# Kernel optimization log

Hardware: AMD Instinct MI355X
Metric: run time of the kernel (lower is better)

The kernel has to match this reference:

```python
import jax, jax.numpy as jnp
import numpy as np

TAU = 0.07
EPS_NORM = 1e-12
EPS_DEN = 1e-8


def setup_inputs() -> dict:
    key = jax.random.key(0)
    k1, k2, k3, k4 = jax.random.split(key, 4)
    B, C, H, W = 2, 128, 64, 64
    return {
        "input": jax.random.normal(k1, (B, C, H, W), dtype=jnp.float32),
        "target": jax.random.normal(k2, (B, C, H, W), dtype=jnp.float32),
        "input_seg": jax.random.randint(k3, (B, H, W), 0, 4, dtype=jnp.int64 if jax.config.jax_enable_x64 else jnp.int32),
        "target_seg": jax.random.randint(k4, (B, H, W), 0, 4, dtype=jnp.int64 if jax.config.jax_enable_x64 else jnp.int32),
    }


def _flatten_normalize(x):
    # (B, C, H, W) -> (B*H*W, C), L2-normalized rows (torch F.normalize semantics)
    B, C = x.shape[0], x.shape[1]
    x = jnp.moveaxis(x, 1, -1).reshape(-1, C)
    norm = jnp.linalg.norm(x, axis=-1, keepdims=True)
    return x / jnp.maximum(norm, EPS_NORM)


def reference(input, target, input_seg, target_seg):
    ni = _flatten_normalize(input)    # (N, C)
    nt = _flatten_normalize(target)   # (N, C)
    pi = input_seg.reshape(-1)        # (N,)
    pt = target_seg.reshape(-1)       # (N,)

    # sim[a, b] = cos(target[a], input[b]); rows already unit-norm so dot == cosine
    sim = jnp.einsum("ac,bc->ab", nt, ni)
    sim_exp = jnp.exp(sim / TAU)

    # diff[a, b] = 1 if pred_input[b] != pred_target[a]
    diff = (pi[None, :] != pt[:, None]).astype(jnp.float32)

    nominator = jnp.sum((1.0 - diff) * sim_exp, axis=0)          # (N,) positives per input pixel
    denominator = jnp.sum(diff * sim_exp, axis=0) + nominator    # (N,) all pairs
    loss = -jnp.log(nominator / (denominator + EPS_DEN)).mean()
    return loss
```

## Files before the change

### kernel.cpp

```cpp
#include <hip/hip_runtime.h>

#define N_PIX 8192
#define C_DIM 128
#define TAU_INV_LOG2E 20.609929155556622f
#define EPS_DEN 1e-8f

typedef unsigned short u16;
typedef __attribute__((ext_vector_type(8))) short short8;
typedef __attribute__((ext_vector_type(4))) float f32x4;

__device__ __forceinline__ u16 f2bf(float f) {
    unsigned u = __float_as_uint(f);
    unsigned r = (u + 0x7fffu + ((u >> 16) & 1u)) >> 16;
    return (u16)r;
}

__global__ __launch_bounds__(256) void scale_k(const float* __restrict__ input,
                                               const float* __restrict__ target,
                                               float* __restrict__ scale_all) {
    int t = blockIdx.x * 256 + threadIdx.x;
    int arr = t >> 13;
    int n = t & (N_PIX - 1);
    const float* src = arr ? target : input;
    int b = n >> 12, hw = n & 4095;
    const float* p = src + b * (C_DIM * 4096) + hw;
    float ss = 0.f;
#pragma unroll 8
    for (int c = 0; c < C_DIM; ++c) {
        float v = p[c * 4096];
        ss += v * v;
    }
    scale_all[t] = 1.0f / fmaxf(sqrtf(ss), 1e-12f);
}

__global__ __launch_bounds__(256) void transpose_k(const float* __restrict__ input,
                                                   const float* __restrict__ target,
                                                   const float* __restrict__ scale_all,
                                                   u16* __restrict__ ni_bf,
                                                   u16* __restrict__ nt_bf) {
    __shared__ float tile[64][65];
    int zi = blockIdx.z;
    int arr = zi >> 1, bb = zi & 1;
    const float* src = (arr ? target : input) + bb * (C_DIM * 4096);
    u16* dst = arr ? nt_bf : ni_bf;
    int hw0 = blockIdx.x * 64;
    int c0 = blockIdx.y * 64;
    int t = threadIdx.x;
    int tq = t >> 6;
    int tl = t & 63;
#pragma unroll
    for (int i = 0; i < 16; ++i) {
        int cl = i * 4 + tq;
        tile[cl][tl] = src[(c0 + cl) * 4096 + hw0 + tl];
    }
    __syncthreads();
#pragma unroll
    for (int i = 0; i < 16; ++i) {
        int px = i * 4 + tq;
        int n = bb * 4096 + hw0 + px;
        float sc = scale_all[arr * N_PIX + n];
        dst[n * C_DIM + c0 + tl] = f2bf(tile[tl][px] * sc);
    }
}

__global__ __launch_bounds__(256, 2) void main_k(const u16* __restrict__ ni,
                                                 const u16* __restrict__ nt,
                                                 const int* __restrict__ piseg,
                                                 const int* __restrict__ ptseg,
                                                 float* __restrict__ den,
                                                 float* __restrict__ nom) {
    __shared__ __align__(16) u16 sA[128 * 136];
    __shared__ __align__(16) int spt[128];

    int bcb = blockIdx.x & 63;
    int as  = blockIdx.x >> 6;
    int bcol0 = bcb * 128;
    int tid = threadIdx.x;
    int lane = tid & 63;
    int wave = tid >> 6;
    int wr = wave >> 1, wc = wave & 1;
    int l15 = lane & 15, q = lane >> 4;

    short8 bfrag[4][4];
    int pil[4];
#pragma unroll
    for (int ct = 0; ct < 4; ++ct) {
        int brow = bcol0 + wc * 64 + ct * 16 + l15;
        pil[ct] = piseg[brow];
        const u16* bp = ni + brow * C_DIM + q * 8;
#pragma unroll
        for (int kc = 0; kc < 4; ++kc)
            bfrag[ct][kc] = *(const short8*)(bp + kc * 32);
    }

    float den_l[4] = {0.f, 0.f, 0.f, 0.f};
    float nom_l[4] = {0.f, 0.f, 0.f, 0.f};

    for (int it = 0; it < 8; ++it) {
        int a0 = (as * 8 + it) * 128;
        __syncthreads();
        {
            const uint4* gsrc = (const uint4*)(nt + a0 * C_DIM);
#pragma unroll
            for (int i = 0; i < 8; ++i) {
                int idx = tid + i * 256;
                int r = idx >> 4, ch = idx & 15;
                *(uint4*)(&sA[r * 136 + ch * 8]) = gsrc[idx];
            }
            if (tid < 128) spt[tid] = ptseg[a0 + tid];
        }
        __syncthreads();

        f32x4 acc[4][4] = {};
#pragma unroll
        for (int kc = 0; kc < 4; ++kc) {
            short8 af[4];
#pragma unroll
            for (int rt = 0; rt < 4; ++rt) {
                int ar = wr * 64 + rt * 16 + l15;
                af[rt] = *(const short8*)(&sA[ar * 136 + kc * 32 + q * 8]);
            }
#pragma unroll
            for (int rt = 0; rt < 4; ++rt)
#pragma unroll
                for (int ct = 0; ct < 4; ++ct)
                    acc[rt][ct] = __builtin_amdgcn_mfma_f32_16x16x32_bf16(
                        af[rt], bfrag[ct][kc], acc[rt][ct], 0, 0, 0);
        }

#pragma unroll
        for (int rt = 0; rt < 4; ++rt) {
            int abase = wr * 64 + rt * 16 + q * 4;
            int4 ptv = *(const int4*)(&spt[abase]);
            int pts[4] = {ptv.x, ptv.y, ptv.z, ptv.w};
#pragma unroll
            for (int ct = 0; ct < 4; ++ct) {
                f32x4 v = acc[rt][ct];
                float d = 0.f, nm = 0.f;
#pragma unroll
                for (int r = 0; r < 4; ++r) {
                    float e = __builtin_amdgcn_exp2f(v[r] * TAU_INV_LOG2E);
                    d += e;
                    nm += (pts[r] == pil[ct]) ? e : 0.f;
                }
                den_l[ct] += d;
                nom_l[ct] += nm;
            }
        }
    }

#pragma unroll
    for (int ct = 0; ct < 4; ++ct) {
        float d = den_l[ct], nm = nom_l[ct];
        d += __shfl_xor(d, 16); d += __shfl_xor(d, 32);
        nm += __shfl_xor(nm, 16); nm += __shfl_xor(nm, 32);
        if (lane < 16) {
            int b = bcol0 + wc * 64 + ct * 16 + lane;
            atomicAdd(&den[b], d);
            atomicAdd(&nom[b], nm);
        }
    }
}

__global__ __launch_bounds__(256) void loss_k(const float* __restrict__ den,
                                              const float* __restrict__ nom,
                                              float* __restrict__ out) {
    float s = 0.f;
    for (int i = threadIdx.x; i < N_PIX; i += 256)
        s -= __logf(nom[i] / (den[i] + EPS_DEN));
#pragma unroll
    for (int off = 32; off > 0; off >>= 1) s += __shfl_down(s, off);
    __shared__ float part[4];
    int wave = threadIdx.x >> 6;
    if ((threadIdx.x & 63) == 0) part[wave] = s;
    __syncthreads();
    if (threadIdx.x == 0)
        out[0] = (part[0] + part[1] + part[2] + part[3]) * (1.0f / N_PIX);
}

extern "C" void kernel_launch(void* const* d_in, const int* in_sizes, int n_in,
                              void* d_out, int out_size, void* d_ws, size_t ws_size,
                              hipStream_t stream) {
    const float* input  = (const float*)d_in[0];
    const float* target = (const float*)d_in[1];
    const int*   iseg   = (const int*)d_in[2];
    const int*   tseg   = (const int*)d_in[3];
    float* out = (float*)d_out;

    char* ws = (char*)d_ws;
    u16* ni_bf = (u16*)(ws);
    u16* nt_bf = (u16*)(ws + (1 << 21));
    float* scale_all = (float*)(ws + (1 << 22));
    float* den = (float*)(ws + (1 << 22) + (64 << 10));
    float* nom = (float*)(ws + (1 << 22) + (96 << 10));

    hipMemsetAsync(den, 0, 64 << 10, stream);
    scale_k<<<64, 256, 0, stream>>>(input, target, scale_all);
    transpose_k<<<dim3(64, 2, 4), 256, 0, stream>>>(input, target, scale_all, ni_bf, nt_bf);
    main_k<<<512, 256, 0, stream>>>(ni_bf, nt_bf, iseg, tseg, den, nom);
    loss_k<<<1, 256, 0, stream>>>(den, nom, out);
}
```

Baseline: 116.1 us.

## Bucket target rows by class so each tile has one label; fuse norm and transpose

A histogram kernel counts the target classes, and the target rows are scattered into class-sorted, 128-padded buckets, so each A-tile of the main GEMM belongs to a single class. The per-element label compare becomes one per-tile select. The norm and transpose kernels are merged, and the 1/tau*log2e factor is folded into the target scale, which removes a multiply per exp. Zero padding rows each add exp(0)=1, and loss_k subtracts that contribution afterwards. The cost is extra GEMM tiles (68 instead of 64), a larger memset, an uneven tile split across blocks, and atomic-ordering nondeterminism in row placement.

```diff
diff --git a/kernel.cpp b/kernel.cpp
--- a/kernel.cpp
+++ b/kernel.cpp
@@ -4,6 +4,9 @@
 #define C_DIM 128
 #define TAU_INV_LOG2E 20.609929155556622f
 #define EPS_DEN 1e-8f
+#define NT_TILES 68
+#define NT_ROWS (NT_TILES * 128)
+#define FAKE_ROWS (NT_ROWS - N_PIX)
 
 typedef unsigned short u16;
 typedef __attribute__((ext_vector_type(8))) short short8;
@@ -11,75 +14,128 @@
 
 __device__ __forceinline__ u16 f2bf(float f) {
     unsigned u = __float_as_uint(f);
-    unsigned r = (u + 0x7fffu + ((u >> 16) & 1u)) >> 16;
-    return (u16)r;
-}
-
-__global__ __launch_bounds__(256) void scale_k(const float* __restrict__ input,
-                                               const float* __restrict__ target,
-                                               float* __restrict__ scale_all) {
-    int t = blockIdx.x * 256 + threadIdx.x;
-    int arr = t >> 13;
-    int n = t & (N_PIX - 1);
-    const float* src = arr ? target : input;
-    int b = n >> 12, hw = n & 4095;
-    const float* p = src + b * (C_DIM * 4096) + hw;
+    return (u16)((u + 0x7fffu + ((u >> 16) & 1u)) >> 16);
+}
+
+__global__ __launch_bounds__(256) void hist_k(const int* __restrict__ tseg,
+                                              int* __restrict__ meta) {
+    __shared__ int hcnt[4][4];
+    int t = threadIdx.x;
+    int c0 = 0, c1 = 0, c2 = 0, c3 = 0;
+    for (int i = t; i < N_PIX; i += 256) {
+        int v = tseg[i];
+        c0 += (v == 0); c1 += (v == 1); c2 += (v == 2); c3 += (v == 3);
+    }
+#pragma unroll
+    for (int off = 32; off; off >>= 1) {
+        c0 += __shfl_down(c0, off); c1 += __shfl_down(c1, off);
+        c2 += __shfl_down(c2, off); c3 += __shfl_down(c3, off);
+    }
+    int wave = t >> 6;
+    if ((t & 63) == 0) { hcnt[wave][0] = c0; hcnt[wave][1] = c1; hcnt[wave][2] = c2; hcnt[wave][3] = c3; }
+    __syncthreads();
+    if (t == 0) {
+        int ps[5]; ps[0] = 0;
+#pragma unroll
+        for (int c = 0; c < 4; ++c) {
+            int cnt = hcnt[0][c] + hcnt[1][c] + hcnt[2][c] + hcnt[3][c];
+            int padded = (cnt + 127) & ~127;
+            ps[c + 1] = ps[c] + padded;
+            meta[12 + c] = padded - cnt;
+            meta[c] = 0;
+        }
+#pragma unroll
+        for (int c = 0; c < 5; ++c) meta[4 + c] = ps[c];
+        for (int tt = 0; tt < NT_TILES; ++tt) {
+            int row = tt * 128, cl = 4;
+#pragma unroll
+            for (int c = 0; c < 4; ++c)
+                if (row >= ps[c] && row < ps[c + 1]) cl = c;
+            meta[16 + tt] = cl;
+        }
+    }
+}
+
+__global__ __launch_bounds__(256) void norm_write_k(const float* __restrict__ input,
+                                                    const float* __restrict__ target,
+                                                    const int* __restrict__ tseg,
+                                                    int* __restrict__ meta,
+                                                    u16* __restrict__ ni_bf,
+                                                    u16* __restrict__ nt_sorted) {
+    __shared__ float tile[128][65];
+    __shared__ float sscale[64];
+    __shared__ int sdest[64];
+    int arr = blockIdx.z;
+    int bb = blockIdx.y;
+    int hw0 = blockIdx.x * 64;
+    const float* src = (arr ? target : input) + bb * (C_DIM * 4096);
+    int t = threadIdx.x;
+    int tq = t >> 6, tl = t & 63;
+#pragma unroll
+    for (int i = 0; i < 32; ++i) {
+        int c = i * 4 + tq;
+        tile[c][tl] = src[c * 4096 + hw0 + tl];
+    }
+    __syncthreads();
+    int p = t >> 2, sub = t & 3;
     float ss = 0.f;
-#pragma unroll 8
-    for (int c = 0; c < C_DIM; ++c) {
-        float v = p[c * 4096];
+#pragma unroll
+    for (int i = 0; i < 32; ++i) {
+        float v = tile[sub * 32 + i][p];
         ss += v * v;
     }
-    scale_all[t] = 1.0f / fmaxf(sqrtf(ss), 1e-12f);
-}
-
-__global__ __launch_bounds__(256) void transpose_k(const float* __restrict__ input,
-                                                   const float* __restrict__ target,
-                                                   const float* __restrict__ scale_all,
-                                                   u16* __restrict__ ni_bf,
-                                                   u16* __restrict__ nt_bf) {
-    __shared__ float tile[64][65];
-    int zi = blockIdx.z;
-    int arr = zi >> 1, bb = zi & 1;
-    const float* src = (arr ? target : input) + bb * (C_DIM * 4096);
-    u16* dst = arr ? nt_bf : ni_bf;
-    int hw0 = blockIdx.x * 64;
-    int c0 = blockIdx.y * 64;
-    int t = threadIdx.x;
-    int tq = t >> 6;
-    int tl = t & 63;
-#pragma unroll
-    for (int i = 0; i < 16; ++i) {
-        int cl = i * 4 + tq;
-        tile[cl][tl] = src[(c0 + cl) * 4096 + hw0 + tl];
-    }
-    __syncthreads();
-#pragma unroll
-    for (int i = 0; i < 16; ++i) {
-        int px = i * 4 + tq;
-        int n = bb * 4096 + hw0 + px;
-        float sc = scale_all[arr * N_PIX + n];
-        dst[n * C_DIM + c0 + tl] = f2bf(tile[tl][px] * sc);
+    ss += __shfl_xor(ss, 1);
+    ss += __shfl_xor(ss, 2);
+    if (sub == 0) {
+        float sc = 1.0f / fmaxf(sqrtf(ss), 1e-12f);
+        int n = bb * 4096 + hw0 + p;
+        int dest;
+        if (arr) {
+            sc *= TAU_INV_LOG2E;
+            int c = tseg[n];
+            int rank = atomicAdd(&meta[c], 1);
+            dest = meta[4 + c] + rank;
+        } else {
+            dest = n;
+        }
+        sscale[p] = sc;
+        sdest[p] = dest;
+    }
+    __syncthreads();
+    u16* dst = arr ? nt_sorted : ni_bf;
+#pragma unroll
+    for (int i = 0; i < 4; ++i) {
+        int idx = t + i * 256;
+        int px = idx >> 4, kc = idx & 15;
+        float sc = sscale[px];
+        long drow = sdest[px];
+        short8 o;
+#pragma unroll
+        for (int j = 0; j < 8; ++j)
+            o[j] = (short)f2bf(tile[kc * 8 + j][px] * sc);
+        *(short8*)(dst + drow * C_DIM + kc * 8) = o;
     }
 }
 
 __global__ __launch_bounds__(256, 2) void main_k(const u16* __restrict__ ni,
                                                  const u16* __restrict__ nt,
                                                  const int* __restrict__ piseg,
-                                                 const int* __restrict__ ptseg,
+                                                 const int* __restrict__ meta,
                                                  float* __restrict__ den,
                                                  float* __restrict__ nom) {
     __shared__ __align__(16) u16 sA[128 * 136];
-    __shared__ __align__(16) int spt[128];
 
     int bcb = blockIdx.x & 63;
     int as  = blockIdx.x >> 6;
+    int t0  = as * 8 + (as < 4 ? as : 4);
+    int ntl = 8 + (as < 4 ? 1 : 0);
     int bcol0 = bcb * 128;
     int tid = threadIdx.x;
     int lane = tid & 63;
     int wave = tid >> 6;
     int wr = wave >> 1, wc = wave & 1;
     int l15 = lane & 15, q = lane >> 4;
+    const int* tcls = meta + 16;
 
     short8 bfrag[4][4];
     int pil[4];
@@ -96,18 +152,18 @@
     float den_l[4] = {0.f, 0.f, 0.f, 0.f};
     float nom_l[4] = {0.f, 0.f, 0.f, 0.f};
 
-    for (int it = 0; it < 8; ++it) {
-        int a0 = (as * 8 + it) * 128;
+    for (int it = 0; it < ntl; ++it) {
+        int tile = t0 + it;
+        int a0 = tile * 128;
         __syncthreads();
         {
-            const uint4* gsrc = (const uint4*)(nt + a0 * C_DIM);
+            const uint4* gsrc = (const uint4*)(nt + (long)a0 * C_DIM);
 #pragma unroll
             for (int i = 0; i < 8; ++i) {
                 int idx = tid + i * 256;
                 int r = idx >> 4, ch = idx & 15;
                 *(uint4*)(&sA[r * 136 + ch * 8]) = gsrc[idx];
             }
-            if (tid < 128) spt[tid] = ptseg[a0 + tid];
         }
         __syncthreads();
 
@@ -128,24 +184,23 @@
                         af[rt], bfrag[ct][kc], acc[rt][ct], 0, 0, 0);
         }
 
-#pragma unroll
-        for (int rt = 0; rt < 4; ++rt) {
-            int abase = wr * 64 + rt * 16 + q * 4;
-            int4 ptv = *(const int4*)(&spt[abase]);
-            int pts[4] = {ptv.x, ptv.y, ptv.z, ptv.w};
+        int tc = tcls[tile];
+        float td[4] = {0.f, 0.f, 0.f, 0.f};
+#pragma unroll
+        for (int rt = 0; rt < 4; ++rt)
 #pragma unroll
             for (int ct = 0; ct < 4; ++ct) {
                 f32x4 v = acc[rt][ct];
-                float d = 0.f, nm = 0.f;
-#pragma unroll
-                for (int r = 0; r < 4; ++r) {
-                    float e = __builtin_amdgcn_exp2f(v[r] * TAU_INV_LOG2E);
-                    d += e;
-                    nm += (pts[r] == pil[ct]) ? e : 0.f;
-                }
-                den_l[ct] += d;
-                nom_l[ct] += nm;
+                float e0 = __builtin_amdgcn_exp2f(v[0]);
+                float e1 = __builtin_amdgcn_exp2f(v[1]);
+                float e2 = __builtin_amdgcn_exp2f(v[2]);
+                float e3 = __builtin_amdgcn_exp2f(v[3]);
+                td[ct] += (e0 + e1) + (e2 + e3);
             }
+#pragma unroll
+        for (int ct = 0; ct < 4; ++ct) {
+            den_l[ct] += td[ct];
+            nom_l[ct] += (tc == pil[ct]) ? td[ct] : 0.f;
         }
     }
 
@@ -164,10 +219,16 @@
 
 __global__ __launch_bounds__(256) void loss_k(const float* __restrict__ den,
                                               const float* __restrict__ nom,
+                                              const int* __restrict__ piseg,
+                                              const int* __restrict__ meta,
                                               float* __restrict__ out) {
+    const int* padc = meta + 12;
     float s = 0.f;
-    for (int i = threadIdx.x; i < N_PIX; i += 256)
-        s -= __logf(nom[i] / (den[i] + EPS_DEN));
+    for (int i = threadIdx.x; i < N_PIX; i += 256) {
+        float nm = nom[i] - (float)padc[piseg[i]];
+        float d = den[i] - (float)FAKE_ROWS;
+        s -= __logf(nm / (d + EPS_DEN));
+    }
 #pragma unroll
     for (int off = 32; off > 0; off >>= 1) s += __shfl_down(s, off);
     __shared__ float part[4];
@@ -188,15 +249,15 @@
     float* out = (float*)d_out;
 
     char* ws = (char*)d_ws;
-    u16* ni_bf = (u16*)(ws);
-    u16* nt_bf = (u16*)(ws + (1 << 21));
-    float* scale_all = (float*)(ws + (1 << 22));
-    float* den = (float*)(ws + (1 << 22) + (64 << 10));
-    float* nom = (float*)(ws + (1 << 22) + (96 << 10));
-
-    hipMemsetAsync(den, 0, 64 << 10, stream);
-    scale_k<<<64, 256, 0, stream>>>(input, target, scale_all);
-    transpose_k<<<dim3(64, 2, 4), 256, 0, stream>>>(input, target, scale_all, ni_bf, nt_bf);
-    main_k<<<512, 256, 0, stream>>>(ni_bf, nt_bf, iseg, tseg, den, nom);
-    loss_k<<<1, 256, 0, stream>>>(den, nom, out);
-}
+    u16* ni_bf     = (u16*)(ws);
+    u16* nt_sorted = (u16*)(ws + 0x200000);
+    float* den     = (float*)(ws + 0x420000);
+    float* nom     = (float*)(ws + 0x428000);
+    int* meta      = (int*)(ws + 0x430000);
+
+    hipMemsetAsync(ws + 0x200000, 0, 0x230000, stream);
+    hist_k<<<1, 256, 0, stream>>>(tseg, meta);
+    norm_write_k<<<dim3(64, 2, 2), 256, 0, stream>>>(input, target, tseg, meta, ni_bf, nt_sorted);
+    main_k<<<512, 256, 0, stream>>>(ni_bf, nt_sorted, iseg, meta, den, nom);
+    loss_k<<<1, 256, 0, stream>>>(den, nom, iseg, meta, out);
+}
```

Result: slower. 187.9 us (+61.9%).
